# Kernel optimization log

Hardware: AMD Instinct MI355X
Metric: run time of the kernel (lower is better)

The kernel has to match this reference:

```python
import jax, jax.numpy as jnp
import numpy as np

S, B, D = 2048, 2, 768
H = 12
R = 64  # adapter bottleneck


def setup_inputs() -> dict:
    key = jax.random.key(0)
    ks = jax.random.split(key, 16)
    d = {
        'query': jax.random.normal(ks[0], (S, B, D), jnp.float32),
        'key':   jax.random.normal(ks[1], (S, B, D), jnp.float32),
        'value': jax.random.normal(ks[2], (S, B, D), jnp.float32),
        'in_proj_w': jax.random.normal(ks[3], (3 * D, D), jnp.float32) * (D ** -0.5),
        'in_proj_b': jax.random.normal(ks[4], (3 * D,), jnp.float32) * 0.02,
        'ssf_scale_1': 1.0 + 0.02 * jax.random.normal(ks[5], (3 * D,), jnp.float32),
        'ssf_shift_1': 0.02 * jax.random.normal(ks[6], (3 * D,), jnp.float32),
        'lora1_down_w': jax.random.normal(ks[7], (R, D), jnp.float32) * (D ** -0.5),
        'lora1_down_b': jnp.zeros((R,), jnp.float32),
        'lora1_up_w': jax.random.normal(ks[8], (3 * D, R), jnp.float32) * 0.02,
        'lora1_up_b': jnp.zeros((3 * D,), jnp.float32),
        'lora1_scale': jnp.ones((1,), jnp.float32),
        'out_w': jax.random.normal(ks[9], (D, D), jnp.float32) * (D ** -0.5),
        'out_b': jnp.zeros((D,), jnp.float32),
        'ssf_scale_2': 1.0 + 0.02 * jax.random.normal(ks[10], (D,), jnp.float32),
        'ssf_shift_2': 0.02 * jax.random.normal(ks[11], (D,), jnp.float32),
        'lora2_down_w': jax.random.normal(ks[12], (R, D), jnp.float32) * (D ** -0.5),
        'lora2_down_b': jnp.zeros((R,), jnp.float32),
        'lora2_up_w': jax.random.normal(ks[13], (D, R), jnp.float32) * 0.02,
        'lora2_up_b': jnp.zeros((D,), jnp.float32),
        'lora2_scale': jnp.ones((1,), jnp.float32),
        'num_heads': H,
    }
    return d


def _adapter(x, dw, db, uw, ub, scale):
    # down -> relu -> up -> * scalar (dropout inactive, add_residual=False)
    h = jax.nn.relu(jnp.einsum('sbd,rd->sbr', x, dw) + db)
    return (jnp.einsum('sbr,er->sbe', h, uw) + ub) * scale[0]


def reference(query, key, value, in_proj_w, in_proj_b, ssf_scale_1, ssf_shift_1,
              lora1_down_w, lora1_down_b, lora1_up_w, lora1_up_b, lora1_scale,
              out_w, out_b, ssf_scale_2, ssf_shift_2,
              lora2_down_w, lora2_down_b, lora2_up_w, lora2_up_b, lora2_scale,
              num_heads):
    tgt, bsz, d = query.shape
    hd = d // num_heads
    scaling = hd ** -0.5
    # fused QKV projection + SSF scale/shift + LoRA adapter on query
    qkv = jnp.einsum('sbd,ed->sbe', query, in_proj_w) + in_proj_b
    qkv = qkv * ssf_scale_1 + ssf_shift_1
    qkv = qkv + _adapter(query, lora1_down_w, lora1_down_b, lora1_up_w, lora1_up_b, lora1_scale)
    q, k, v = jnp.split(qkv, 3, axis=-1)
    q = q * scaling
    # [S,B,D] -> [B*H, S, hd]
    def to_heads(t):
        return t.reshape(tgt, bsz * num_heads, hd).transpose(1, 0, 2)
    q, k, v = to_heads(q), to_heads(k), to_heads(v)
    attn = jax.nn.softmax(jnp.einsum('nqh,nkh->nqk', q, k), axis=-1)
    out = jnp.einsum('nqk,nkh->nqh', attn, v)  # [B*H, S, hd]
    out = out.transpose(1, 0, 2).reshape(tgt, bsz, d)
    # lora2 on pre-projection attn output
    ad2 = _adapter(out, lora2_down_w, lora2_down_b, lora2_up_w, lora2_up_b, lora2_scale)
    o = jnp.einsum('sbd,ed->sbe', out, out_w) + out_b
    o = o * ssf_scale_2 + ssf_shift_2
    return o + ad2
```

## Files before the change

kernel.cpp:

```cpp
#include <hip/hip_runtime.h>
#include <stdint.h>

typedef float f32x4 __attribute__((ext_vector_type(4)));
typedef _Float16 f16x8 __attribute__((ext_vector_type(8)));
typedef _Float16 f16x4 __attribute__((ext_vector_type(4)));
typedef unsigned int u32x2 __attribute__((ext_vector_type(2)));

#define MFMAH(a, b, c)  __builtin_amdgcn_mfma_f32_16x16x32_f16(a, b, c, 0, 0, 0)
#define MFMAH16(a, b, c) __builtin_amdgcn_mfma_f32_16x16x16f16(a, b, c, 0, 0, 0)

#define GLOAD16(gp, lp) __builtin_amdgcn_global_load_lds( \
    (__attribute__((address_space(1))) void*)(void*)(gp), \
    (__attribute__((address_space(3))) void*)(void*)(lp), 16, 0, 0)

#define QSCALE (0.125f * 1.44269504f)
#define SMOFF 8.0f

static __device__ inline f32x4 zero4() { f32x4 z; z[0]=0.f; z[1]=0.f; z[2]=0.f; z[3]=0.f; return z; }

static __device__ inline unsigned int pk2(float a, float b) {
  return __builtin_bit_cast(unsigned int, __builtin_amdgcn_cvt_pkrtz(a, b));
}

__global__ void k_pre(const float* __restrict__ s0, const float* __restrict__ s1,
                      const float* __restrict__ s2, const float* __restrict__ s3,
                      const float* __restrict__ s4,
                      _Float16* __restrict__ d0, _Float16* __restrict__ d1,
                      _Float16* __restrict__ d2, _Float16* __restrict__ d3,
                      _Float16* __restrict__ d4,
                      int n0, int n1, int n2, int n3, int n4,
                      const float* __restrict__ uw1, const float* __restrict__ sc1,
                      const float* __restrict__ lsc1, _Float16* __restrict__ up1,
                      const float* __restrict__ uw2, const float* __restrict__ sc2,
                      const float* __restrict__ lsc2, _Float16* __restrict__ up2,
                      const float* __restrict__ b1, const float* __restrict__ sh1,
                      const float* __restrict__ ub1, float* __restrict__ c1,
                      const float* __restrict__ b2, const float* __restrict__ sh2,
                      const float* __restrict__ ub2, float* __restrict__ c2) {
  int gid = blockIdx.x*blockDim.x + threadIdx.x;
  if (gid < 2304*64) up1[gid] = (_Float16)(uw1[gid] * lsc1[0] / sc1[gid >> 6]);
  if (gid < 768*64)  up2[gid] = (_Float16)(uw2[gid] * lsc2[0] / sc2[gid >> 6]);
  if (gid < 2304)    c1[gid] = sc1[gid]*b1[gid] + sh1[gid] + lsc1[0]*ub1[gid];
  if (gid < 768)     c2[gid] = sc2[gid]*b2[gid] + sh2[gid] + lsc2[0]*ub2[gid];
  int total = n0 + n1 + n2 + n3 + n4;
  for (int i = gid; i < total; i += gridDim.x*blockDim.x) {
    const float* src; _Float16* dst; int j = i;
    if (j < n0) { src = s0; dst = d0; }
    else { j -= n0;
      if (j < n1) { src = s1; dst = d1; }
      else { j -= n1;
        if (j < n2) { src = s2; dst = d2; }
        else { j -= n2;
          if (j < n3) { src = s3; dst = d3; }
          else { j -= n3; src = s4; dst = d4; }
        }
      }
    }
    float4 v = ((const float4*)src)[j];
    f16x4 o;
    o[0] = (_Float16)v.x; o[1] = (_Float16)v.y; o[2] = (_Float16)v.z; o[3] = (_Float16)v.w;
    ((f16x4*)dst)[j] = o;
  }
}

__global__ __launch_bounds__(256) void k_lora_h(const _Float16* __restrict__ A,
    const _Float16* __restrict__ Dw, const float* __restrict__ db, _Float16* __restrict__ H) {
  const int wave = threadIdx.x >> 6, lane = threadIdx.x & 63;
  const int g = lane >> 4, li = lane & 15;
  const int rowbase = blockIdx.x * 16;
  f32x4 acc = zero4();
  for (int k0 = 0; k0 < 768; k0 += 32) {
    f16x8 a = *(const f16x8*)(A + (size_t)(rowbase + li)*768 + k0 + g*8);
    f16x8 b = *(const f16x8*)(Dw + (size_t)(wave*16 + li)*768 + k0 + g*8);
    acc = MFMAH(a, b, acc);
  }
  int r = wave*16 + li;
  float bias = db[r];
  #pragma unroll
  for (int j = 0; j < 4; j++) {
    float v = acc[j] + bias;
    H[(size_t)(rowbase + g*4 + j)*64 + r] = (_Float16)fmaxf(v, 0.f);
  }
}

template<int EPI>
__global__ __launch_bounds__(256) void k_gemm(
    const _Float16* __restrict__ A, const _Float16* __restrict__ B,
    const _Float16* __restrict__ Ha, const _Float16* __restrict__ Up,
    const float* __restrict__ Sc, const float* __restrict__ Cst,
    float* __restrict__ Cout, _Float16* __restrict__ qh,
    _Float16* __restrict__ kh, _Float16* __restrict__ vT) {
  __shared__ _Float16 lsA[2][4096];
  __shared__ _Float16 lsB[2][4096];
  const int wave = threadIdx.x >> 6, lane = threadIdx.x & 63;
  const int g = lane >> 4, li = lane & 15;
  const int wr = wave >> 1, wc = wave & 1;
  const int rb = blockIdx.x * 128, cb = blockIdx.y * 128;

  f32x4 acc[4][4];
  #pragma unroll
  for (int m = 0; m < 4; m++)
    #pragma unroll
    for (int n = 0; n < 4; n++) acc[m][n] = zero4();

  auto stage = [&](int buf, int k0) {
    #pragma unroll
    for (int c = 0; c < 2; c++) {
      int p = (wave*2 + c)*64 + lane;
      int r = p >> 2, cp = p & 3;
      int cc = (cp - (r >> 1)) & 3;
      GLOAD16(A + (size_t)(rb + r)*768 + k0 + cc*8, &lsA[buf][(wave*2 + c)*512]);
      GLOAD16(B + (size_t)(cb + r)*768 + k0 + cc*8, &lsB[buf][(wave*2 + c)*512]);
    }
  };

  stage(0, 0);
  __syncthreads();
  int cur = 0;
  for (int t = 0; t < 24; t++) {
    if (t + 1 < 24) stage(cur ^ 1, (t + 1) * 32);
    f16x8 ah[4], bh[4];
    #pragma unroll
    for (int m = 0; m < 4; m++) {
      int row = wr*64 + m*16 + li;
      int cp = (g + (row >> 1)) & 3;
      ah[m] = *(const f16x8*)(&lsA[cur][row*32 + cp*8]);
    }
    #pragma unroll
    for (int n = 0; n < 4; n++) {
      int row = wc*64 + n*16 + li;
      int cp = (g + (row >> 1)) & 3;
      bh[n] = *(const f16x8*)(&lsB[cur][row*32 + cp*8]);
    }
    __builtin_amdgcn_s_setprio(1);
    #pragma unroll
    for (int m = 0; m < 4; m++)
      #pragma unroll
      for (int n = 0; n < 4; n++)
        acc[m][n] = MFMAH(ah[m], bh[n], acc[m][n]);
    __builtin_amdgcn_s_setprio(0);
    __syncthreads();
    cur ^= 1;
  }

  _Float16* l0a = &lsA[0][0];
  _Float16* l0b = &lsB[0][0];
  #pragma unroll
  for (int c = 0; c < 4; c++) {
    int p = (wave*4 + c)*64 + lane;
    int r = p >> 3, cp = p & 7;
    int cc = (cp - r) & 7;
    GLOAD16(Ha + (size_t)(rb + r)*64 + cc*8, l0a + (wave*4 + c)*512);
    GLOAD16(Up + (size_t)(cb + r)*64 + cc*8, l0b + (wave*4 + c)*512);
  }
  __syncthreads();
  #pragma unroll
  for (int s = 0; s < 2; s++) {
    f16x8 ha[4], ub[4];
    #pragma unroll
    for (int m = 0; m < 4; m++) {
      int row = wr*64 + m*16 + li;
      int cp = ((s*4 + g) + row) & 7;
      ha[m] = *(const f16x8*)(l0a + row*64 + cp*8);
    }
    #pragma unroll
    for (int n = 0; n < 4; n++) {
      int row = wc*64 + n*16 + li;
      int cp = ((s*4 + g) + row) & 7;
      ub[n] = *(const f16x8*)(l0b + row*64 + cp*8);
    }
    #pragma unroll
    for (int m = 0; m < 4; m++)
      #pragma unroll
      for (int n = 0; n < 4; n++)
        acc[m][n] = MFMAH(ha[m], ub[n], acc[m][n]);
  }

  #pragma unroll
  for (int n = 0; n < 4; n++) {
    int col = cb + wc*64 + n*16 + li;
    float sc = Sc[col], ct = Cst[col];
    #pragma unroll
    for (int m = 0; m < 4; m++) {
      #pragma unroll
      for (int j = 0; j < 4; j++) {
        int row = rb + wr*64 + m*16 + g*4 + j;
        float v = sc * acc[m][n][j] + ct;
        if (EPI == 0) {
          Cout[(size_t)row*768 + col] = v;
        } else {
          int sect = col / 768;
          int eh = col - sect*768;
          int hh = eh >> 6, hd = eh & 63;
          int si = row >> 1, bb = row & 1;
          int nh = bb*12 + hh;
          if (sect == 0)      qh[((size_t)nh*2048 + si)*64 + hd] = (_Float16)(v * QSCALE);
          else if (sect == 1) kh[((size_t)nh*2048 + si)*64 + hd] = (_Float16)v;
          else                vT[((size_t)nh*64 + hd)*2048 + si] = (_Float16)v;
        }
      }
    }
  }
}

__global__ __launch_bounds__(256, 3) void k_attn(const _Float16* __restrict__ qh,
    const _Float16* __restrict__ kh, const _Float16* __restrict__ vT,
    _Float16* __restrict__ outf) {
  const int wave = threadIdx.x >> 6, lane = threadIdx.x & 63;
  const int g = lane >> 4, li = lane & 15;
  const int head = blockIdx.x;
  const int q0 = blockIdx.y*64;
  const _Float16* Qb = qh + (size_t)head*2048*64;
  const _Float16* Kb = kh + (size_t)head*2048*64;
  const _Float16* Vb = vT + (size_t)head*64*2048;
  __shared__ char smem[36864];
  _Float16* Kt = (_Float16*)smem;
  _Float16* Vt = (_Float16*)(smem + 16384);

  auto stage = [&](int buf, int kb) {
    #pragma unroll
    for (int c = 0; c < 2; c++) {
      int idx = c*256 + wave*64 + lane;
      int r = idx >> 3, cp = idx & 7;
      int csrc = cp ^ (r & 7);
      GLOAD16(Kb + (size_t)(kb + r)*64 + csrc*8, Kt + buf*4096 + (c*256 + wave*64)*8);
      GLOAD16(Vb + (size_t)r*2048 + kb + csrc*8, Vt + buf*4096 + (c*256 + wave*64)*8);
    }
  };

  f16x8 qf[4][2];
  #pragma unroll
  for (int ct = 0; ct < 4; ct++)
    #pragma unroll
    for (int dw = 0; dw < 2; dw++)
      qf[ct][dw] = *(const f16x8*)(Qb + (size_t)(q0 + 16*ct + li)*64 + dw*32 + g*8);

  f32x4 o[4][4];
  #pragma unroll
  for (int dt = 0; dt < 4; dt++)
    #pragma unroll
    for (int qt = 0; qt < 4; qt++) o[dt][qt] = zero4();
  float sj[4] = {0.f, 0.f, 0.f, 0.f};
  const int sw = li & 7;

  stage(0, 0);
  __syncthreads();
  int cur = 0;
  for (int t = 0; t < 32; t++) {
    if (t + 1 < 32) stage(cur ^ 1, (t + 1) * 64);
    const _Float16* Kl = Kt + cur*4096;
    const _Float16* Vl = Vt + cur*4096;
    const int krow = 16*wave + li;
    f16x8 kf0 = *(const f16x8*)(Kl + krow*64 + (g ^ sw)*8);
    f16x8 kf1 = *(const f16x8*)(Kl + krow*64 + ((4 + g) ^ sw)*8);
    f32x4 c[4];
    __builtin_amdgcn_s_setprio(1);
    #pragma unroll
    for (int ct = 0; ct < 4; ct++) {
      c[ct][0] = -SMOFF; c[ct][1] = -SMOFF; c[ct][2] = -SMOFF; c[ct][3] = -SMOFF;
      c[ct] = MFMAH(kf0, qf[ct][0], c[ct]);
      c[ct] = MFMAH(kf1, qf[ct][1], c[ct]);
    }
    __builtin_amdgcn_s_setprio(0);
    f16x4 pf[4];
    #pragma unroll
    for (int ct = 0; ct < 4; ct++) {
      float p0 = __builtin_amdgcn_exp2f(c[ct][0]);
      float p1 = __builtin_amdgcn_exp2f(c[ct][1]);
      float p2 = __builtin_amdgcn_exp2f(c[ct][2]);
      float p3 = __builtin_amdgcn_exp2f(c[ct][3]);
      sj[ct] += (p0 + p1) + (p2 + p3);
      u32x2 pk; pk[0] = pk2(p0, p1); pk[1] = pk2(p2, p3);
      pf[ct] = __builtin_bit_cast(f16x4, pk);
    }
    __builtin_amdgcn_s_setprio(1);
    #pragma unroll
    for (int dt = 0; dt < 4; dt++) {
      const int drow = 16*dt + li;
      const _Float16* va = Vl + drow*64 + (((2*wave + (g >> 1)) ^ sw)*8) + 4*(g & 1);
      f16x4 vf = *(const f16x4*)va;
      #pragma unroll
      for (int qt = 0; qt < 4; qt++)
        o[dt][qt] = MFMAH16(vf, pf[qt], o[dt][qt]);
    }
    __builtin_amdgcn_s_setprio(0);
    __syncthreads();
    cur ^= 1;
  }

  _Float16* part = (_Float16*)smem;
  float* lrp = (float*)(smem + 32768);
  #pragma unroll
  for (int dt = 0; dt < 4; dt++)
    #pragma unroll
    for (int qt = 0; qt < 4; qt++) {
      u32x2 pw;
      pw[0] = pk2(o[dt][qt][0], o[dt][qt][1]);
      pw[1] = pk2(o[dt][qt][2], o[dt][qt][3]);
      *(u32x2*)(part + ((wave*16 + dt*4 + qt)*64 + lane)*4) = pw;
    }
  #pragma unroll
  for (int ct = 0; ct < 4; ct++) {
    float a = sj[ct];
    a += __shfl_xor(a, 16);
    a += __shfl_xor(a, 32);
    lrp[(wave*4 + ct)*64 + lane] = a;
  }
  __syncthreads();
  const int bb = head / 12, hh = head % 12;
  #pragma unroll
  for (int qt = 0; qt < 4; qt++) {
    float lr = lrp[qt*64 + lane] + lrp[(4 + qt)*64 + lane]
             + lrp[(8 + qt)*64 + lane] + lrp[(12 + qt)*64 + lane];
    float inv = 1.f / lr;
    float s0 = 0.f, s1 = 0.f, s2 = 0.f, s3 = 0.f;
    #pragma unroll
    for (int p = 0; p < 4; p++) {
      f16x4 pv = *(const f16x4*)(part + ((p*16 + wave*4 + qt)*64 + lane)*4);
      s0 += (float)pv[0]; s1 += (float)pv[1]; s2 += (float)pv[2]; s3 += (float)pv[3];
    }
    const int si = q0 + 16*qt + li;
    f16x4 ov;
    ov[0] = (_Float16)(s0 * inv); ov[1] = (_Float16)(s1 * inv);
    ov[2] = (_Float16)(s2 * inv); ov[3] = (_Float16)(s3 * inv);
    *(f16x4*)(&outf[((size_t)si*2 + bb)*768 + hh*64 + 16*wave + 4*g]) = ov;
  }
}

extern "C" void kernel_launch(void* const* d_in, const int* in_sizes, int n_in,
                              void* d_out, int out_size, void* d_ws, size_t ws_size,
                              hipStream_t stream) {
  (void)in_sizes; (void)n_in; (void)out_size; (void)ws_size;
  const float* query = (const float*)d_in[0];
  const float* w1   = (const float*)d_in[3];
  const float* b1   = (const float*)d_in[4];
  const float* s1   = (const float*)d_in[5];
  const float* sh1  = (const float*)d_in[6];
  const float* dw1  = (const float*)d_in[7];
  const float* db1  = (const float*)d_in[8];
  const float* uw1  = (const float*)d_in[9];
  const float* ub1  = (const float*)d_in[10];
  const float* lsc1 = (const float*)d_in[11];
  const float* w2   = (const float*)d_in[12];
  const float* b2   = (const float*)d_in[13];
  const float* s2   = (const float*)d_in[14];
  const float* sh2  = (const float*)d_in[15];
  const float* dw2  = (const float*)d_in[16];
  const float* db2  = (const float*)d_in[17];
  const float* uw2  = (const float*)d_in[18];
  const float* ub2  = (const float*)d_in[19];
  const float* lsc2 = (const float*)d_in[20];
  float* out = (float*)d_out;

  char* ws = (char*)d_ws;
  size_t off = 0;
  auto alloc = [&](size_t bytes) -> char* {
    char* p = ws + off; off += (bytes + 255) & ~(size_t)255; return p;
  };
  typedef _Float16 F16;
  F16* qf16 = (F16*)alloc((size_t)4096*768*2);
  F16* w1f  = (F16*)alloc((size_t)2304*768*2);
  F16* w2f  = (F16*)alloc((size_t)768*768*2);
  F16* d1f  = (F16*)alloc((size_t)64*768*2);
  F16* d2f  = (F16*)alloc((size_t)64*768*2);
  F16* up1p = (F16*)alloc((size_t)2304*64*2);
  F16* up2p = (F16*)alloc((size_t)768*64*2);
  float* c1 = (float*)alloc((size_t)2304*4);
  float* c2 = (float*)alloc((size_t)768*4);
  F16* h1   = (F16*)alloc((size_t)4096*64*2);
  F16* h2   = (F16*)alloc((size_t)4096*64*2);
  F16* qhd  = (F16*)alloc((size_t)24*2048*64*2);
  F16* khd  = (F16*)alloc((size_t)24*2048*64*2);
  F16* vTd  = (F16*)alloc((size_t)24*64*2048*2);
  F16* of16 = (F16*)alloc((size_t)4096*768*2);

  k_pre<<<2048, 256, 0, stream>>>(query, w1, w2, dw1, dw2,
                                  qf16, w1f, w2f, d1f, d2f,
                                  4096*768/4, 2304*768/4, 768*768/4,
                                  64*768/4, 64*768/4,
                                  uw1, s1, lsc1, up1p, uw2, s2, lsc2, up2p,
                                  b1, sh1, ub1, c1, b2, sh2, ub2, c2);
  k_lora_h<<<256, 256, 0, stream>>>(qf16, d1f, db1, h1);
  k_gemm<1><<<dim3(32, 18), 256, 0, stream>>>(qf16, w1f, h1, up1p, s1, c1,
                                              nullptr, qhd, khd, vTd);
  k_attn<<<dim3(24, 32), 256, 0, stream>>>(qhd, khd, vTd, of16);
  k_lora_h<<<256, 256, 0, stream>>>(of16, d2f, db2, h2);
  k_gemm<0><<<dim3(32, 6), 256, 0, stream>>>(of16, w2f, h2, up2p, s2, c2,
                                             out, nullptr, nullptr, nullptr);
}
```

Measured before the change: 115.2 us.

## Split-K the LoRA down kernel and narrow GEMM column tiles

The LoRA down-projection kernel now splits K across its four waves. Each wave computes all four 16-column tiles over a 192-wide K slice, and the partials are reduced through shared memory. This lets A fragments be reused across column tiles and shortens the serial MFMA chain per wave. The GEMM's column tile shrinks from 128 to 96 with a launch-bounds occupancy hint, which raises the block count (32x24 and 32x8) to fill more CUs. In exchange there is lower per-block MFMA reuse, plus an extra sync and LDS round trip in the LoRA kernel.

```diff
diff --git a/kernel.cpp b/kernel.cpp
--- a/kernel.cpp
+++ b/kernel.cpp
@@ -68,49 +68,67 @@
   const int wave = threadIdx.x >> 6, lane = threadIdx.x & 63;
   const int g = lane >> 4, li = lane & 15;
   const int rowbase = blockIdx.x * 16;
-  f32x4 acc = zero4();
-  for (int k0 = 0; k0 < 768; k0 += 32) {
-    f16x8 a = *(const f16x8*)(A + (size_t)(rowbase + li)*768 + k0 + g*8);
-    f16x8 b = *(const f16x8*)(Dw + (size_t)(wave*16 + li)*768 + k0 + g*8);
-    acc = MFMAH(a, b, acc);
+  __shared__ f32x4 part[4][4][64];
+  f32x4 acc[4];
+  #pragma unroll
+  for (int nt = 0; nt < 4; nt++) acc[nt] = zero4();
+  const int kbase = wave * 192;
+  for (int k0 = 0; k0 < 192; k0 += 32) {
+    f16x8 a = *(const f16x8*)(A + (size_t)(rowbase + li)*768 + kbase + k0 + g*8);
+    #pragma unroll
+    for (int nt = 0; nt < 4; nt++) {
+      f16x8 b = *(const f16x8*)(Dw + (size_t)(nt*16 + li)*768 + kbase + k0 + g*8);
+      acc[nt] = MFMAH(a, b, acc[nt]);
+    }
+  }
+  #pragma unroll
+  for (int nt = 0; nt < 4; nt++) part[wave][nt][lane] = acc[nt];
+  __syncthreads();
+  f32x4 s = part[0][wave][lane];
+  #pragma unroll
+  for (int p = 1; p < 4; p++) {
+    f32x4 t = part[p][wave][lane];
+    s[0] += t[0]; s[1] += t[1]; s[2] += t[2]; s[3] += t[3];
   }
   int r = wave*16 + li;
   float bias = db[r];
   #pragma unroll
   for (int j = 0; j < 4; j++) {
-    float v = acc[j] + bias;
+    float v = s[j] + bias;
     H[(size_t)(rowbase + g*4 + j)*64 + r] = (_Float16)fmaxf(v, 0.f);
   }
 }
 
 template<int EPI>
-__global__ __launch_bounds__(256) void k_gemm(
+__global__ __launch_bounds__(256, 3) void k_gemm(
     const _Float16* __restrict__ A, const _Float16* __restrict__ B,
     const _Float16* __restrict__ Ha, const _Float16* __restrict__ Up,
     const float* __restrict__ Sc, const float* __restrict__ Cst,
     float* __restrict__ Cout, _Float16* __restrict__ qh,
     _Float16* __restrict__ kh, _Float16* __restrict__ vT) {
   __shared__ _Float16 lsA[2][4096];
-  __shared__ _Float16 lsB[2][4096];
-  const int wave = threadIdx.x >> 6, lane = threadIdx.x & 63;
+  __shared__ _Float16 lsB[2][3072];
+  const int tid = threadIdx.x;
+  const int wave = tid >> 6, lane = tid & 63;
   const int g = lane >> 4, li = lane & 15;
   const int wr = wave >> 1, wc = wave & 1;
-  const int rb = blockIdx.x * 128, cb = blockIdx.y * 128;
-
-  f32x4 acc[4][4];
+  const int rb = blockIdx.x * 128, cb = blockIdx.y * 96;
+
+  f32x4 acc[4][3];
   #pragma unroll
   for (int m = 0; m < 4; m++)
     #pragma unroll
-    for (int n = 0; n < 4; n++) acc[m][n] = zero4();
+    for (int n = 0; n < 3; n++) acc[m][n] = zero4();
 
   auto stage = [&](int buf, int k0) {
     #pragma unroll
     for (int c = 0; c < 2; c++) {
-      int p = (wave*2 + c)*64 + lane;
+      int p = c*256 + tid;
       int r = p >> 2, cp = p & 3;
       int cc = (cp - (r >> 1)) & 3;
-      GLOAD16(A + (size_t)(rb + r)*768 + k0 + cc*8, &lsA[buf][(wave*2 + c)*512]);
-      GLOAD16(B + (size_t)(cb + r)*768 + k0 + cc*8, &lsB[buf][(wave*2 + c)*512]);
+      GLOAD16(A + (size_t)(rb + r)*768 + k0 + cc*8, &lsA[buf][(c*256 + wave*64)*8]);
+      if (c == 0 || tid < 128)
+        GLOAD16(B + (size_t)(cb + r)*768 + k0 + cc*8, &lsB[buf][(c*256 + wave*64)*8]);
     }
   };
 
@@ -119,7 +137,7 @@
   int cur = 0;
   for (int t = 0; t < 24; t++) {
     if (t + 1 < 24) stage(cur ^ 1, (t + 1) * 32);
-    f16x8 ah[4], bh[4];
+    f16x8 ah[4], bh[3];
     #pragma unroll
     for (int m = 0; m < 4; m++) {
       int row = wr*64 + m*16 + li;
@@ -127,8 +145,8 @@
       ah[m] = *(const f16x8*)(&lsA[cur][row*32 + cp*8]);
     }
     #pragma unroll
-    for (int n = 0; n < 4; n++) {
-      int row = wc*64 + n*16 + li;
+    for (int n = 0; n < 3; n++) {
+      int row = wc*48 + n*16 + li;
       int cp = (g + (row >> 1)) & 3;
       bh[n] = *(const f16x8*)(&lsB[cur][row*32 + cp*8]);
     }
@@ -136,7 +154,7 @@
     #pragma unroll
     for (int m = 0; m < 4; m++)
       #pragma unroll
-      for (int n = 0; n < 4; n++)
+      for (int n = 0; n < 3; n++)
         acc[m][n] = MFMAH(ah[m], bh[n], acc[m][n]);
     __builtin_amdgcn_s_setprio(0);
     __syncthreads();
@@ -147,16 +165,17 @@
   _Float16* l0b = &lsB[0][0];
   #pragma unroll
   for (int c = 0; c < 4; c++) {
-    int p = (wave*4 + c)*64 + lane;
+    int p = c*256 + tid;
     int r = p >> 3, cp = p & 7;
     int cc = (cp - r) & 7;
-    GLOAD16(Ha + (size_t)(rb + r)*64 + cc*8, l0a + (wave*4 + c)*512);
-    GLOAD16(Up + (size_t)(cb + r)*64 + cc*8, l0b + (wave*4 + c)*512);
+    GLOAD16(Ha + (size_t)(rb + r)*64 + cc*8, l0a + (c*256 + wave*64)*8);
+    if (c < 3)
+      GLOAD16(Up + (size_t)(cb + r)*64 + cc*8, l0b + (c*256 + wave*64)*8);
   }
   __syncthreads();
   #pragma unroll
   for (int s = 0; s < 2; s++) {
-    f16x8 ha[4], ub[4];
+    f16x8 ha[4], ub[3];
     #pragma unroll
     for (int m = 0; m < 4; m++) {
       int row = wr*64 + m*16 + li;
@@ -164,21 +183,21 @@
       ha[m] = *(const f16x8*)(l0a + row*64 + cp*8);
     }
     #pragma unroll
-    for (int n = 0; n < 4; n++) {
-      int row = wc*64 + n*16 + li;
+    for (int n = 0; n < 3; n++) {
+      int row = wc*48 + n*16 + li;
       int cp = ((s*4 + g) + row) & 7;
       ub[n] = *(const f16x8*)(l0b + row*64 + cp*8);
     }
     #pragma unroll
     for (int m = 0; m < 4; m++)
       #pragma unroll
-      for (int n = 0; n < 4; n++)
+      for (int n = 0; n < 3; n++)
         acc[m][n] = MFMAH(ha[m], ub[n], acc[m][n]);
   }
 
   #pragma unroll
-  for (int n = 0; n < 4; n++) {
-    int col = cb + wc*64 + n*16 + li;
+  for (int n = 0; n < 3; n++) {
+    int col = cb + wc*48 + n*16 + li;
     float sc = Sc[col], ct = Cst[col];
     #pragma unroll
     for (int m = 0; m < 4; m++) {
@@ -381,10 +400,10 @@
                                   uw1, s1, lsc1, up1p, uw2, s2, lsc2, up2p,
                                   b1, sh1, ub1, c1, b2, sh2, ub2, c2);
   k_lora_h<<<256, 256, 0, stream>>>(qf16, d1f, db1, h1);
-  k_gemm<1><<<dim3(32, 18), 256, 0, stream>>>(qf16, w1f, h1, up1p, s1, c1,
+  k_gemm<1><<<dim3(32, 24), 256, 0, stream>>>(qf16, w1f, h1, up1p, s1, c1,
                                               nullptr, qhd, khd, vTd);
   k_attn<<<dim3(24, 32), 256, 0, stream>>>(qhd, khd, vTd, of16);
   k_lora_h<<<256, 256, 0, stream>>>(of16, d2f, db2, h2);
-  k_gemm<0><<<dim3(32, 6), 256, 0, stream>>>(of16, w2f, h2, up2p, s2, c2,
+  k_gemm<0><<<dim3(32, 8), 256, 0, stream>>>(of16, w2f, h2, up2p, s2, c2,
                                              out, nullptr, nullptr, nullptr);
 }
```

After: 104.5 us, median of 2. 1.1x faster.
